# Kernel tuning notes

Hardware: AMD Instinct MI355X
Metric: run time of the kernel (lower is better)

Reference implementation:

```python
import jax, jax.numpy as jnp
import numpy as np

N = 500_000      # num nodes
E = 8_000_000    # num edges (before self-loops)
F_IN, H, C = 16, 8, 2


def setup_inputs() -> dict:
    key = jax.random.key(0)
    k = jax.random.split(key, 6)
    x = jax.random.normal(k[0], (N, F_IN), dtype=jnp.float32)
    edge_index = jax.random.randint(k[1], (2, E), 0, N, dtype=jnp.int32)
    # Glorot-style init like PyG GCNConv
    W1 = jax.random.normal(k[2], (F_IN, H), dtype=jnp.float32) * (1.0 / np.sqrt(F_IN))
    b1 = jnp.zeros((H,), dtype=jnp.float32)
    W2 = jax.random.normal(k[3], (H, C), dtype=jnp.float32) * (1.0 / np.sqrt(H))
    b2 = jnp.zeros((C,), dtype=jnp.float32)
    return {"x": x, "W1": W1, "b1": b1, "W2": W2, "b2": b2, "edge_index": edge_index}


def reference(x, W1, b1, W2, b2, edge_index):
    # GCNConv: out = D^{-1/2} (A + I) D^{-1/2} X W + b   (PyG semantics)
    row, col = edge_index[0], edge_index[1]           # messages flow row -> col
    loop = jnp.arange(N, dtype=row.dtype)
    row = jnp.concatenate([row, loop])                # add self-loops
    col = jnp.concatenate([col, loop])
    deg = jax.ops.segment_sum(jnp.ones_like(col, dtype=x.dtype), col, num_segments=N)
    dinv = jnp.where(deg > 0, jax.lax.rsqrt(deg), jnp.zeros_like(deg))
    norm = dinv[row] * dinv[col]                      # [E+N]

    def propagate(h):  # h: [N, d] -> normalized scatter-add aggregation
        msg = h[row] * norm[:, None]                  # gather + scale, [E+N, d]
        return jax.ops.segment_sum(msg, col, num_segments=N)

    h = jax.nn.relu(propagate(x @ W1) + b1)           # [N, 8]
    out = propagate(h @ W2) + b2                      # [N, 2]
    return jax.nn.log_softmax(out, axis=1)
```

## Files before the change

kernel.cpp:

```cpp
#include <hip/hip_runtime.h>

#define TPB 256
#define NBLK_EDGE 1024
#define CHUNKE 8192
#define BIN_SHIFT 9
#define BIN_SIZE 512
#define MAXK 1024
#define ROW_BITS 19
#define ROW_MASK ((1u << ROW_BITS) - 1)
#define Q_SHIFT 17
#define NKEY 2048
#define CAP 12288

typedef _Float16 half8  __attribute__((ext_vector_type(8)));
typedef _Float16 half2v __attribute__((ext_vector_type(2)));

__global__ void k_hist(const int* __restrict__ col, int E, int chunk, int K,
                       int* __restrict__ cntB, int* __restrict__ cntT) {
    __shared__ int lh[MAXK];
    int blk = blockIdx.x;
    for (int k = threadIdx.x; k < MAXK; k += blockDim.x) lh[k] = 0;
    __syncthreads();
    int s = blk * chunk, e_ = min(s + chunk, E);
    for (int e = s + threadIdx.x; e < e_; e += blockDim.x)
        atomicAdd(&lh[col[e] >> BIN_SHIFT], 1);
    __syncthreads();
    for (int k = threadIdx.x; k < MAXK; k += blockDim.x) {
        int v = lh[k];
        cntB[(size_t)blk * MAXK + k] = v;
        cntT[(size_t)k * NBLK_EDGE + blk] = v;
    }
}

__global__ void k_colscan(int* __restrict__ cntT, int* __restrict__ ghist) {
    __shared__ int part[256];
    int b = blockIdx.x, tid = threadIdx.x;
    size_t base = (size_t)b * NBLK_EDGE;
    int t4 = tid * 4;
    int c0 = cntT[base + t4], c1 = cntT[base + t4 + 1],
        c2 = cntT[base + t4 + 2], c3 = cntT[base + t4 + 3];
    int sum = c0 + c1 + c2 + c3;
    part[tid] = sum;
    __syncthreads();
    for (int off = 1; off < 256; off <<= 1) {
        int v = (tid >= off) ? part[tid - off] : 0;
        __syncthreads();
        part[tid] += v;
        __syncthreads();
    }
    int excl = part[tid] - sum;
    cntT[base + t4]     = excl;
    cntT[base + t4 + 1] = excl + c0;
    cntT[base + t4 + 2] = excl + c0 + c1;
    cntT[base + t4 + 3] = excl + c0 + c1 + c2;
    if (tid == 255) ghist[b] = part[255];
}

__global__ void k_scan(const int* __restrict__ ghist, int K, int* __restrict__ binBase,
                       int* __restrict__ scratchCur) {
    __shared__ int tmp[MAXK];
    int tid = threadIdx.x;
    if (tid == 0) *scratchCur = 0;
    int val = (tid < K) ? ghist[tid] : 0;
    tmp[tid] = val;
    __syncthreads();
    for (int off = 1; off < MAXK; off <<= 1) {
        int v = (tid >= off) ? tmp[tid - off] : 0;
        __syncthreads();
        tmp[tid] += v;
        __syncthreads();
    }
    int incl = tmp[tid];
    if (tid < K) binBase[tid] = incl - val;
    if (tid == K - 1) binBase[K] = incl;
}

__global__ void __launch_bounds__(1024) k_reorder(
        const int* __restrict__ row, const int* __restrict__ col,
        int E, int chunk, int K,
        const int* __restrict__ binBase, const int* __restrict__ cntB,
        const int* __restrict__ cntT, unsigned* __restrict__ packed) {
    __shared__ unsigned sorted[CHUNKE];
    __shared__ unsigned short sbin[CHUNKE];
    __shared__ int lcur[MAXK], lbase[MAXK], gbase[MAXK];
    __shared__ int part[1024];
    int blk = blockIdx.x, tid = threadIdx.x;
    int s = blk * chunk, e_ = min(s + chunk, E), len = e_ - s;
    size_t bb = (size_t)blk * MAXK;
    int c0 = cntB[bb + tid];
    part[tid] = c0;
    __syncthreads();
    for (int off = 1; off < 1024; off <<= 1) {
        int v = (tid >= off) ? part[tid - off] : 0;
        __syncthreads();
        part[tid] += v;
        __syncthreads();
    }
    int excl = part[tid] - c0;
    lbase[tid] = excl;
    lcur[tid] = excl;
    gbase[tid] = binBase[tid] + cntT[(size_t)tid * NBLK_EDGE + blk];
    __syncthreads();
    for (int i = tid; i < len; i += blockDim.x) {
        int cc = col[s + i];
        int b = cc >> BIN_SHIFT;
        int slot = atomicAdd(&lcur[b], 1);
        sorted[slot] = ((unsigned)(cc & (BIN_SIZE - 1)) << ROW_BITS) | (unsigned)row[s + i];
        sbin[slot] = (unsigned short)b;
    }
    __syncthreads();
    for (int i = tid; i < len; i += blockDim.x) {
        int b = sbin[i];
        packed[gbase[b] + (i - lbase[b])] = sorted[i];
    }
}

__global__ void __launch_bounds__(1024) k_binsort_deg(
        unsigned* __restrict__ packed, const int* __restrict__ binBase,
        unsigned* __restrict__ scratch, int* __restrict__ scratchCur,
        const float* __restrict__ x, const float* __restrict__ W1,
        float* __restrict__ dinv, half8* __restrict__ g0,
        int* __restrict__ keyptr, int N, int E, int K) {
    __shared__ unsigned buf2[CAP];
    __shared__ int cnt[NKEY], cur[NKEY];
    __shared__ int part[1024];
    __shared__ int sbShared;
    int tid = threadIdx.x;
    int bin = blockIdx.x;
    int s = binBase[bin], t = binBase[bin + 1];
    int len = t - s;
    bool fast = (len <= CAP);
    cnt[tid] = 0;
    cnt[tid + 1024] = 0;
    if (!fast && tid == 0) sbShared = atomicAdd(scratchCur, len);
    __syncthreads();
    for (int i = tid; i < len; i += blockDim.x) {
        unsigned v = packed[s + i];
        int k = (int)((v >> ROW_BITS) << 2) | (int)((v & ROW_MASK) >> Q_SHIFT);
        atomicAdd(&cnt[k], 1);
    }
    __syncthreads();
    int t2 = tid * 2;
    int c0 = cnt[t2], c1 = cnt[t2 + 1];
    int sum = c0 + c1;
    part[tid] = sum;
    __syncthreads();
    for (int off = 1; off < 1024; off <<= 1) {
        int v = (tid >= off) ? part[tid - off] : 0;
        __syncthreads();
        part[tid] += v;
        __syncthreads();
    }
    int excl = part[tid] - sum;
    cur[t2] = excl;
    cur[t2 + 1] = excl + c0;
    int base = bin << BIN_SHIFT;
    if (base + (t2 >> 2) < N) keyptr[((size_t)bin << 11) + t2] = s + excl;
    if (base + ((t2 + 1) >> 2) < N) keyptr[((size_t)bin << 11) + t2 + 1] = s + excl + c0;
    float di = 0.0f;
    int node = base + tid;
    if (tid < BIN_SIZE && node < N) {
        int deg = cnt[4 * tid] + cnt[4 * tid + 1] + cnt[4 * tid + 2] + cnt[4 * tid + 3];
        di = rsqrtf((float)(deg + 1));
        dinv[node] = di;
    }
    if (bin == K - 1 && tid == 0) keyptr[(size_t)4 * N] = E;
    __syncthreads();
    if (fast) {
        for (int i = tid; i < len; i += blockDim.x) {
            unsigned v = packed[s + i];
            int k = (int)((v >> ROW_BITS) << 2) | (int)((v & ROW_MASK) >> Q_SHIFT);
            int slot = atomicAdd(&cur[k], 1);
            buf2[slot] = v;
        }
        __syncthreads();
        for (int i = tid; i < len; i += blockDim.x) packed[s + i] = buf2[i];
    } else {
        unsigned* stg = scratch + sbShared;
        for (int i = tid; i < len; i += blockDim.x) stg[i] = packed[s + i];
        __threadfence();
        __syncthreads();
        for (int i = tid; i < len; i += blockDim.x) {
            unsigned v = stg[i];
            int k = (int)((v >> ROW_BITS) << 2) | (int)((v & ROW_MASK) >> Q_SHIFT);
            int slot = atomicAdd(&cur[k], 1);
            packed[s + slot] = v;
        }
    }
    if (tid < BIN_SIZE && node < N) {
        const float4* xv = (const float4*)(x + (size_t)node * 16);
        float h[8];
#pragma unroll
        for (int j = 0; j < 8; ++j) h[j] = 0.0f;
#pragma unroll
        for (int kk = 0; kk < 4; ++kk) {
            float4 a = xv[kk];
            int kb = kk * 4;
#pragma unroll
            for (int j = 0; j < 8; ++j)
                h[j] += a.x * W1[kb * 8 + j] + a.y * W1[(kb + 1) * 8 + j]
                      + a.z * W1[(kb + 2) * 8 + j] + a.w * W1[(kb + 3) * 8 + j];
        }
        half8 g;
#pragma unroll
        for (int j = 0; j < 8; ++j) g[j] = (_Float16)(di * h[j]);
        g0[node] = g;
    }
}

__global__ void k_gather1_phase(const unsigned* __restrict__ packed,
                                const int* __restrict__ keyptr,
                                const half8* __restrict__ g0,
                                const float* __restrict__ dinv_arr,
                                const float* __restrict__ b1,
                                const float* __restrict__ W2,
                                float* __restrict__ accA,
                                half2v* __restrict__ g1, int N, int q) {
    int i = blockIdx.x * blockDim.x + threadIdx.x;
    if (i >= N) return;
    int s = keyptr[4 * i + q], t = keyptr[4 * i + q + 1];
    float acc[8];
    if (q == 0) {
#pragma unroll
        for (int j = 0; j < 8; ++j) acc[j] = 0.0f;
    } else {
        const float4* av = (const float4*)(accA + (size_t)i * 8);
        float4 lo = av[0], hi = av[1];
        acc[0] = lo.x; acc[1] = lo.y; acc[2] = lo.z; acc[3] = lo.w;
        acc[4] = hi.x; acc[5] = hi.y; acc[6] = hi.z; acc[7] = hi.w;
    }
    int e = s;
    for (; e + 4 <= t; e += 4) {
        unsigned p0 = packed[e], p1 = packed[e + 1], p2 = packed[e + 2], p3 = packed[e + 3];
        half8 v0 = g0[p0 & ROW_MASK];
        half8 v1 = g0[p1 & ROW_MASK];
        half8 v2 = g0[p2 & ROW_MASK];
        half8 v3 = g0[p3 & ROW_MASK];
#pragma unroll
        for (int j = 0; j < 8; ++j)
            acc[j] += (float)v0[j] + (float)v1[j] + (float)v2[j] + (float)v3[j];
    }
    for (; e < t; ++e) {
        half8 v = g0[packed[e] & ROW_MASK];
#pragma unroll
        for (int j = 0; j < 8; ++j) acc[j] += (float)v[j];
    }
    if (q < 3) {
        float4* av = (float4*)(accA + (size_t)i * 8);
        av[0] = make_float4(acc[0], acc[1], acc[2], acc[3]);
        av[1] = make_float4(acc[4], acc[5], acc[6], acc[7]);
    } else {
        half8 self = g0[i];
        float di = dinv_arr[i];
        float o0 = 0.0f, o1 = 0.0f;
#pragma unroll
        for (int j = 0; j < 8; ++j) {
            float hj = fmaxf(di * (acc[j] + (float)self[j]) + b1[j], 0.0f);
            o0 += hj * W2[j * 2 + 0];
            o1 += hj * W2[j * 2 + 1];
        }
        half2v g;
        g.x = (_Float16)(di * o0);
        g.y = (_Float16)(di * o1);
        g1[i] = g;
    }
}

__global__ void k_gather2_final(const unsigned* __restrict__ packed,
                                const int* __restrict__ keyptr,
                                const half2v* __restrict__ g1,
                                const float* __restrict__ dinv_arr,
                                const float* __restrict__ b2,
                                float* __restrict__ out, int N) {
    int i = blockIdx.x * blockDim.x + threadIdx.x;
    if (i >= N) return;
    int s = keyptr[4 * i], t = keyptr[4 * i + 4];
    half2v sg = g1[i];
    float a0 = (float)sg.x, a1 = (float)sg.y;
    int e = s;
    for (; e + 4 <= t; e += 4) {
        unsigned p0 = packed[e], p1 = packed[e + 1], p2 = packed[e + 2], p3 = packed[e + 3];
        half2v v0 = g1[p0 & ROW_MASK];
        half2v v1 = g1[p1 & ROW_MASK];
        half2v v2 = g1[p2 & ROW_MASK];
        half2v v3 = g1[p3 & ROW_MASK];
        a0 += (float)v0.x + (float)v1.x + (float)v2.x + (float)v3.x;
        a1 += (float)v0.y + (float)v1.y + (float)v2.y + (float)v3.y;
    }
    for (; e < t; ++e) {
        half2v v = g1[packed[e] & ROW_MASK];
        a0 += (float)v.x;
        a1 += (float)v.y;
    }
    float di = dinv_arr[i];
    float o0 = di * a0 + b2[0];
    float o1 = di * a1 + b2[1];
    float m = fmaxf(o0, o1);
    float lse = m + logf(expf(o0 - m) + expf(o1 - m));
    ((float2*)out)[i] = make_float2(o0 - lse, o1 - lse);
}

extern "C" void kernel_launch(void* const* d_in, const int* in_sizes, int n_in,
                              void* d_out, int out_size, void* d_ws, size_t ws_size,
                              hipStream_t stream) {
    const float* x  = (const float*)d_in[0];
    const float* W1 = (const float*)d_in[1];
    const float* b1 = (const float*)d_in[2];
    const float* W2 = (const float*)d_in[3];
    const float* b2 = (const float*)d_in[4];
    const int*   ei = (const int*)d_in[5];

    const int N = in_sizes[0] / 16;
    const int E = in_sizes[5] / 2;
    const int* row = ei;
    const int* col = ei + E;
    const int K = (N + BIN_SIZE - 1) >> BIN_SHIFT;

    float* ws   = (float*)d_ws;
    float* dinv = ws;
    half8* g0   = (half8*)(ws + (size_t)N);
    half2v* g1  = (half2v*)(ws + (size_t)5 * N);
    float* accA = ws + (size_t)6 * N;
    int* keyptr = (int*)(ws + (size_t)14 * N);
    int*   meta = (int*)(ws + (size_t)18 * N + 8);
    int* ghist      = meta;
    int* binBase    = meta + MAXK;
    int* scratchCur = meta + 2 * MAXK + 16;
    unsigned* packed = (unsigned*)(meta + 3 * MAXK);
    int* cntB = (int*)(packed + E);
    int* cntT = cntB + (size_t)MAXK * NBLK_EDGE;

    float* out = (float*)d_out;

    const int gN = (N + TPB - 1) / TPB;
    const int chunk = (E + NBLK_EDGE - 1) / NBLK_EDGE;

    k_hist       <<<NBLK_EDGE, TPB, 0, stream>>>(col, E, chunk, K, cntB, cntT);
    k_colscan    <<<K, 256, 0, stream>>>(cntT, ghist);
    k_scan       <<<1, MAXK, 0, stream>>>(ghist, K, binBase, scratchCur);
    k_reorder    <<<NBLK_EDGE, 1024, 0, stream>>>(row, col, E, chunk, K,
                                                  binBase, cntB, cntT, packed);
    k_binsort_deg<<<K, 1024, 0, stream>>>(packed, binBase, (unsigned*)accA, scratchCur,
                                          x, W1, dinv, g0, keyptr, N, E, K);
    for (int q = 0; q < 4; ++q)
        k_gather1_phase<<<gN, TPB, 0, stream>>>(packed, keyptr, g0, dinv, b1, W2,
                                                accA, g1, N, q);
    k_gather2_final<<<gN, TPB, 0, stream>>>(packed, keyptr, g1, dinv, b2, out, N);
}
```

Measured before the change: 371.9 us.

## Fuse gather phases, recompute dinv from keyptr, use wave-shuffle scans

The four per-quarter gather1 launches become one kernel that walks all four row-range segments in sequence. A __syncthreads between segments keeps threads of a block working on the same quarter of g0, which preserves some locality. The accA round-trip and the dinv array are removed, and dinv is recomputed from the keyptr span. Block scans now use wave shuffles instead of shared-memory Hillis-Steele, W1 is staged in LDS, and the edge chunking changes to 512 blocks of 1024 threads. The main risk is that the phase-wise cache locality the separate launches gave may weaken without a grid-wide barrier.

```diff
diff --git a/kernel.cpp b/kernel.cpp
--- a/kernel.cpp
+++ b/kernel.cpp
@@ -1,8 +1,8 @@
 #include <hip/hip_runtime.h>
 
 #define TPB 256
-#define NBLK_EDGE 1024
-#define CHUNKE 8192
+#define NBLK_EDGE 512
+#define CHUNKE 16384
 #define BIN_SHIFT 9
 #define BIN_SIZE 512
 #define MAXK 1024
@@ -15,31 +15,56 @@
 typedef _Float16 half8  __attribute__((ext_vector_type(8)));
 typedef _Float16 half2v __attribute__((ext_vector_type(2)));
 
-__global__ void k_hist(const int* __restrict__ col, int E, int chunk, int K,
-                       int* __restrict__ cntB, int* __restrict__ cntT) {
+__device__ __forceinline__ int wave_scan_incl(int v, int lane) {
+#pragma unroll
+    for (int d = 1; d < 64; d <<= 1) {
+        int u = __shfl_up(v, d, 64);
+        if (lane >= d) v += u;
+    }
+    return v;
+}
+
+__device__ __forceinline__ int block_excl_scan_1024(int v, int tid, int* wsum) {
+    int lane = tid & 63, wv = tid >> 6;
+    int incl = wave_scan_incl(v, lane);
+    if (lane == 63) wsum[wv] = incl;
+    __syncthreads();
+    if (tid < 16) {
+        int w = wsum[tid];
+#pragma unroll
+        for (int d = 1; d < 16; d <<= 1) {
+            int u = __shfl_up(w, d, 16);
+            if (tid >= d) w += u;
+        }
+        wsum[tid] = w;
+    }
+    __syncthreads();
+    return incl - v + (wv ? wsum[wv - 1] : 0);
+}
+
+__global__ void __launch_bounds__(1024) k_hist(
+        const int* __restrict__ col, int E, int chunk,
+        int* __restrict__ cntB, int* __restrict__ cntT) {
     __shared__ int lh[MAXK];
-    int blk = blockIdx.x;
-    for (int k = threadIdx.x; k < MAXK; k += blockDim.x) lh[k] = 0;
+    int blk = blockIdx.x, tid = threadIdx.x;
+    lh[tid] = 0;
     __syncthreads();
     int s = blk * chunk, e_ = min(s + chunk, E);
-    for (int e = s + threadIdx.x; e < e_; e += blockDim.x)
+    for (int e = s + tid; e < e_; e += 1024)
         atomicAdd(&lh[col[e] >> BIN_SHIFT], 1);
     __syncthreads();
-    for (int k = threadIdx.x; k < MAXK; k += blockDim.x) {
-        int v = lh[k];
-        cntB[(size_t)blk * MAXK + k] = v;
-        cntT[(size_t)k * NBLK_EDGE + blk] = v;
-    }
+    int v = lh[tid];
+    cntB[(size_t)blk * MAXK + tid] = v;
+    cntT[(size_t)tid * NBLK_EDGE + blk] = v;
 }
 
 __global__ void k_colscan(int* __restrict__ cntT, int* __restrict__ ghist) {
     __shared__ int part[256];
     int b = blockIdx.x, tid = threadIdx.x;
     size_t base = (size_t)b * NBLK_EDGE;
-    int t4 = tid * 4;
-    int c0 = cntT[base + t4], c1 = cntT[base + t4 + 1],
-        c2 = cntT[base + t4 + 2], c3 = cntT[base + t4 + 3];
-    int sum = c0 + c1 + c2 + c3;
+    int t2 = tid * 2;
+    int c0 = cntT[base + t2], c1 = cntT[base + t2 + 1];
+    int sum = c0 + c1;
     part[tid] = sum;
     __syncthreads();
     for (int off = 1; off < 256; off <<= 1) {
@@ -49,54 +74,37 @@
         __syncthreads();
     }
     int excl = part[tid] - sum;
-    cntT[base + t4]     = excl;
-    cntT[base + t4 + 1] = excl + c0;
-    cntT[base + t4 + 2] = excl + c0 + c1;
-    cntT[base + t4 + 3] = excl + c0 + c1 + c2;
+    cntT[base + t2]     = excl;
+    cntT[base + t2 + 1] = excl + c0;
     if (tid == 255) ghist[b] = part[255];
 }
 
-__global__ void k_scan(const int* __restrict__ ghist, int K, int* __restrict__ binBase,
-                       int* __restrict__ scratchCur) {
-    __shared__ int tmp[MAXK];
+__global__ void __launch_bounds__(1024) k_scan(
+        const int* __restrict__ ghist, int K, int* __restrict__ binBase,
+        int* __restrict__ scratchCur) {
+    __shared__ int wsum[16];
     int tid = threadIdx.x;
     if (tid == 0) *scratchCur = 0;
     int val = (tid < K) ? ghist[tid] : 0;
-    tmp[tid] = val;
-    __syncthreads();
-    for (int off = 1; off < MAXK; off <<= 1) {
-        int v = (tid >= off) ? tmp[tid - off] : 0;
-        __syncthreads();
-        tmp[tid] += v;
-        __syncthreads();
-    }
-    int incl = tmp[tid];
-    if (tid < K) binBase[tid] = incl - val;
-    if (tid == K - 1) binBase[K] = incl;
+    int excl = block_excl_scan_1024(val, tid, wsum);
+    binBase[tid] = excl;
+    if (tid == K - 1) binBase[K] = excl + val;
 }
 
 __global__ void __launch_bounds__(1024) k_reorder(
         const int* __restrict__ row, const int* __restrict__ col,
-        int E, int chunk, int K,
+        int E, int chunk,
         const int* __restrict__ binBase, const int* __restrict__ cntB,
         const int* __restrict__ cntT, unsigned* __restrict__ packed) {
     __shared__ unsigned sorted[CHUNKE];
     __shared__ unsigned short sbin[CHUNKE];
     __shared__ int lcur[MAXK], lbase[MAXK], gbase[MAXK];
-    __shared__ int part[1024];
+    __shared__ int wsum[16];
     int blk = blockIdx.x, tid = threadIdx.x;
     int s = blk * chunk, e_ = min(s + chunk, E), len = e_ - s;
     size_t bb = (size_t)blk * MAXK;
     int c0 = cntB[bb + tid];
-    part[tid] = c0;
-    __syncthreads();
-    for (int off = 1; off < 1024; off <<= 1) {
-        int v = (tid >= off) ? part[tid - off] : 0;
-        __syncthreads();
-        part[tid] += v;
-        __syncthreads();
-    }
-    int excl = part[tid] - c0;
+    int excl = block_excl_scan_1024(c0, tid, wsum);
     lbase[tid] = excl;
     lcur[tid] = excl;
     gbase[tid] = binBase[tid] + cntT[(size_t)tid * NBLK_EDGE + blk];
@@ -115,15 +123,15 @@
     }
 }
 
-__global__ void __launch_bounds__(1024) k_binsort_deg(
+__global__ void __launch_bounds__(1024) k_binsort(
         unsigned* __restrict__ packed, const int* __restrict__ binBase,
         unsigned* __restrict__ scratch, int* __restrict__ scratchCur,
         const float* __restrict__ x, const float* __restrict__ W1,
-        float* __restrict__ dinv, half8* __restrict__ g0,
-        int* __restrict__ keyptr, int N, int E, int K) {
+        half8* __restrict__ g0, int* __restrict__ keyptr, int N, int E, int K) {
     __shared__ unsigned buf2[CAP];
     __shared__ int cnt[NKEY], cur[NKEY];
-    __shared__ int part[1024];
+    __shared__ float w1s[128];
+    __shared__ int wsum[16];
     __shared__ int sbShared;
     int tid = threadIdx.x;
     int bin = blockIdx.x;
@@ -132,9 +140,10 @@
     bool fast = (len <= CAP);
     cnt[tid] = 0;
     cnt[tid + 1024] = 0;
+    if (tid < 128) w1s[tid] = W1[tid];
     if (!fast && tid == 0) sbShared = atomicAdd(scratchCur, len);
     __syncthreads();
-    for (int i = tid; i < len; i += blockDim.x) {
+    for (int i = tid; i < len; i += 1024) {
         unsigned v = packed[s + i];
         int k = (int)((v >> ROW_BITS) << 2) | (int)((v & ROW_MASK) >> Q_SHIFT);
         atomicAdd(&cnt[k], 1);
@@ -142,16 +151,7 @@
     __syncthreads();
     int t2 = tid * 2;
     int c0 = cnt[t2], c1 = cnt[t2 + 1];
-    int sum = c0 + c1;
-    part[tid] = sum;
-    __syncthreads();
-    for (int off = 1; off < 1024; off <<= 1) {
-        int v = (tid >= off) ? part[tid - off] : 0;
-        __syncthreads();
-        part[tid] += v;
-        __syncthreads();
-    }
-    int excl = part[tid] - sum;
+    int excl = block_excl_scan_1024(c0 + c1, tid, wsum);
     cur[t2] = excl;
     cur[t2 + 1] = excl + c0;
     int base = bin << BIN_SHIFT;
@@ -162,25 +162,24 @@
     if (tid < BIN_SIZE && node < N) {
         int deg = cnt[4 * tid] + cnt[4 * tid + 1] + cnt[4 * tid + 2] + cnt[4 * tid + 3];
         di = rsqrtf((float)(deg + 1));
-        dinv[node] = di;
     }
     if (bin == K - 1 && tid == 0) keyptr[(size_t)4 * N] = E;
     __syncthreads();
     if (fast) {
-        for (int i = tid; i < len; i += blockDim.x) {
+        for (int i = tid; i < len; i += 1024) {
             unsigned v = packed[s + i];
             int k = (int)((v >> ROW_BITS) << 2) | (int)((v & ROW_MASK) >> Q_SHIFT);
             int slot = atomicAdd(&cur[k], 1);
             buf2[slot] = v;
         }
         __syncthreads();
-        for (int i = tid; i < len; i += blockDim.x) packed[s + i] = buf2[i];
+        for (int i = tid; i < len; i += 1024) packed[s + i] = buf2[i];
     } else {
         unsigned* stg = scratch + sbShared;
-        for (int i = tid; i < len; i += blockDim.x) stg[i] = packed[s + i];
+        for (int i = tid; i < len; i += 1024) stg[i] = packed[s + i];
         __threadfence();
         __syncthreads();
-        for (int i = tid; i < len; i += blockDim.x) {
+        for (int i = tid; i < len; i += 1024) {
             unsigned v = stg[i];
             int k = (int)((v >> ROW_BITS) << 2) | (int)((v & ROW_MASK) >> Q_SHIFT);
             int slot = atomicAdd(&cur[k], 1);
@@ -198,8 +197,8 @@
             int kb = kk * 4;
 #pragma unroll
             for (int j = 0; j < 8; ++j)
-                h[j] += a.x * W1[kb * 8 + j] + a.y * W1[(kb + 1) * 8 + j]
-                      + a.z * W1[(kb + 2) * 8 + j] + a.w * W1[(kb + 3) * 8 + j];
+                h[j] += a.x * w1s[kb * 8 + j] + a.y * w1s[(kb + 1) * 8 + j]
+                      + a.z * w1s[(kb + 2) * 8 + j] + a.w * w1s[(kb + 3) * 8 + j];
         }
         half8 g;
 #pragma unroll
@@ -208,50 +207,48 @@
     }
 }
 
-__global__ void k_gather1_phase(const unsigned* __restrict__ packed,
-                                const int* __restrict__ keyptr,
-                                const half8* __restrict__ g0,
-                                const float* __restrict__ dinv_arr,
-                                const float* __restrict__ b1,
-                                const float* __restrict__ W2,
-                                float* __restrict__ accA,
-                                half2v* __restrict__ g1, int N, int q) {
+__global__ void __launch_bounds__(TPB) k_gather1(
+        const unsigned* __restrict__ packed, const int* __restrict__ keyptr,
+        const half8* __restrict__ g0, const float* __restrict__ b1,
+        const float* __restrict__ W2, half2v* __restrict__ g1, int N) {
     int i = blockIdx.x * blockDim.x + threadIdx.x;
-    if (i >= N) return;
-    int s = keyptr[4 * i + q], t = keyptr[4 * i + q + 1];
+    bool act = (i < N);
+    int kp0 = 0, kp1 = 0, kp2 = 0, kp3 = 0, kp4 = 0;
+    if (act) {
+        int4 k4 = ((const int4*)keyptr)[i];
+        kp0 = k4.x; kp1 = k4.y; kp2 = k4.z; kp3 = k4.w;
+        kp4 = keyptr[4 * i + 4];
+    }
     float acc[8];
-    if (q == 0) {
-#pragma unroll
-        for (int j = 0; j < 8; ++j) acc[j] = 0.0f;
-    } else {
-        const float4* av = (const float4*)(accA + (size_t)i * 8);
-        float4 lo = av[0], hi = av[1];
-        acc[0] = lo.x; acc[1] = lo.y; acc[2] = lo.z; acc[3] = lo.w;
-        acc[4] = hi.x; acc[5] = hi.y; acc[6] = hi.z; acc[7] = hi.w;
-    }
-    int e = s;
-    for (; e + 4 <= t; e += 4) {
-        unsigned p0 = packed[e], p1 = packed[e + 1], p2 = packed[e + 2], p3 = packed[e + 3];
-        half8 v0 = g0[p0 & ROW_MASK];
-        half8 v1 = g0[p1 & ROW_MASK];
-        half8 v2 = g0[p2 & ROW_MASK];
-        half8 v3 = g0[p3 & ROW_MASK];
-#pragma unroll
-        for (int j = 0; j < 8; ++j)
-            acc[j] += (float)v0[j] + (float)v1[j] + (float)v2[j] + (float)v3[j];
-    }
-    for (; e < t; ++e) {
-        half8 v = g0[packed[e] & ROW_MASK];
-#pragma unroll
-        for (int j = 0; j < 8; ++j) acc[j] += (float)v[j];
-    }
-    if (q < 3) {
-        float4* av = (float4*)(accA + (size_t)i * 8);
-        av[0] = make_float4(acc[0], acc[1], acc[2], acc[3]);
-        av[1] = make_float4(acc[4], acc[5], acc[6], acc[7]);
-    } else {
+#pragma unroll
+    for (int j = 0; j < 8; ++j) acc[j] = 0.0f;
+#pragma unroll
+    for (int q = 0; q < 4; ++q) {
+        int e = (q == 0) ? kp0 : (q == 1) ? kp1 : (q == 2) ? kp2 : kp3;
+        int t = (q == 0) ? kp1 : (q == 1) ? kp2 : (q == 2) ? kp3 : kp4;
+        if (act) {
+            for (; e + 4 <= t; e += 4) {
+                unsigned p0 = packed[e], p1 = packed[e + 1],
+                         p2 = packed[e + 2], p3 = packed[e + 3];
+                half8 v0 = g0[p0 & ROW_MASK];
+                half8 v1 = g0[p1 & ROW_MASK];
+                half8 v2 = g0[p2 & ROW_MASK];
+                half8 v3 = g0[p3 & ROW_MASK];
+#pragma unroll
+                for (int j = 0; j < 8; ++j)
+                    acc[j] += (float)v0[j] + (float)v1[j] + (float)v2[j] + (float)v3[j];
+            }
+            for (; e < t; ++e) {
+                half8 v = g0[packed[e] & ROW_MASK];
+#pragma unroll
+                for (int j = 0; j < 8; ++j) acc[j] += (float)v[j];
+            }
+        }
+        __syncthreads();
+    }
+    if (act) {
         half8 self = g0[i];
-        float di = dinv_arr[i];
+        float di = rsqrtf((float)(kp4 - kp0 + 1));
         float o0 = 0.0f, o1 = 0.0f;
 #pragma unroll
         for (int j = 0; j < 8; ++j) {
@@ -266,12 +263,10 @@
     }
 }
 
-__global__ void k_gather2_final(const unsigned* __restrict__ packed,
-                                const int* __restrict__ keyptr,
-                                const half2v* __restrict__ g1,
-                                const float* __restrict__ dinv_arr,
-                                const float* __restrict__ b2,
-                                float* __restrict__ out, int N) {
+__global__ void __launch_bounds__(TPB) k_gather2(
+        const unsigned* __restrict__ packed, const int* __restrict__ keyptr,
+        const half2v* __restrict__ g1, const float* __restrict__ b2,
+        float* __restrict__ out, int N) {
     int i = blockIdx.x * blockDim.x + threadIdx.x;
     if (i >= N) return;
     int s = keyptr[4 * i], t = keyptr[4 * i + 4];
@@ -292,7 +287,7 @@
         a0 += (float)v.x;
         a1 += (float)v.y;
     }
-    float di = dinv_arr[i];
+    float di = rsqrtf((float)(t - s + 1));
     float o0 = di * a0 + b2[0];
     float o1 = di * a1 + b2[1];
     float m = fmaxf(o0, o1);
@@ -317,12 +312,11 @@
     const int K = (N + BIN_SIZE - 1) >> BIN_SHIFT;
 
     float* ws   = (float*)d_ws;
-    float* dinv = ws;
-    half8* g0   = (half8*)(ws + (size_t)N);
-    half2v* g1  = (half2v*)(ws + (size_t)5 * N);
-    float* accA = ws + (size_t)6 * N;
-    int* keyptr = (int*)(ws + (size_t)14 * N);
-    int*   meta = (int*)(ws + (size_t)18 * N + 8);
+    half8* g0   = (half8*)ws;
+    half2v* g1  = (half2v*)(ws + (size_t)4 * N);
+    unsigned* scratch = (unsigned*)(ws + (size_t)5 * N);
+    int* keyptr = (int*)(ws + (size_t)13 * N);
+    int*   meta = (int*)(ws + (size_t)17 * N + 8);
     int* ghist      = meta;
     int* binBase    = meta + MAXK;
     int* scratchCur = meta + 2 * MAXK + 16;
@@ -335,15 +329,13 @@
     const int gN = (N + TPB - 1) / TPB;
     const int chunk = (E + NBLK_EDGE - 1) / NBLK_EDGE;
 
-    k_hist       <<<NBLK_EDGE, TPB, 0, stream>>>(col, E, chunk, K, cntB, cntT);
-    k_colscan    <<<K, 256, 0, stream>>>(cntT, ghist);
-    k_scan       <<<1, MAXK, 0, stream>>>(ghist, K, binBase, scratchCur);
-    k_reorder    <<<NBLK_EDGE, 1024, 0, stream>>>(row, col, E, chunk, K,
-                                                  binBase, cntB, cntT, packed);
-    k_binsort_deg<<<K, 1024, 0, stream>>>(packed, binBase, (unsigned*)accA, scratchCur,
-                                          x, W1, dinv, g0, keyptr, N, E, K);
-    for (int q = 0; q < 4; ++q)
-        k_gather1_phase<<<gN, TPB, 0, stream>>>(packed, keyptr, g0, dinv, b1, W2,
-                                                accA, g1, N, q);
-    k_gather2_final<<<gN, TPB, 0, stream>>>(packed, keyptr, g1, dinv, b2, out, N);
-}
+    k_hist   <<<NBLK_EDGE, 1024, 0, stream>>>(col, E, chunk, cntB, cntT);
+    k_colscan<<<K, 256, 0, stream>>>(cntT, ghist);
+    k_scan   <<<1, MAXK, 0, stream>>>(ghist, K, binBase, scratchCur);
+    k_reorder<<<NBLK_EDGE, 1024, 0, stream>>>(row, col, E, chunk,
+                                              binBase, cntB, cntT, packed);
+    k_binsort<<<K, 1024, 0, stream>>>(packed, binBase, scratch, scratchCur,
+                                      x, W1, g0, keyptr, N, E, K);
+    k_gather1<<<gN, TPB, 0, stream>>>(packed, keyptr, g0, b1, W2, g1, N);
+    k_gather2<<<gN, TPB, 0, stream>>>(packed, keyptr, g1, b2, out, N);
+}
```

After: 351.2 us. 5.6% less time.
